# Kernel tuning notes

Measured on AMD Instinct MI355X. Metric: run time of the kernel, lower is better.

Reference implementation:

```python
import jax, jax.numpy as jnp
import numpy as np

NUM_HEADS = 8
HEAD_DIM = 64
HIDDEN_SIZE = 128
TOP_K = 16
EPS = 1e-6


def setup_inputs() -> dict:
    key = jax.random.key(0)
    k1, k2, k3 = jax.random.split(key, 3)
    B, H, S, D = 4, NUM_HEADS, 1024, HEAD_DIM
    return {
        "keys": jax.random.normal(k1, (B, H, S, D), dtype=jnp.float32),
        "values": jax.random.normal(k2, (B, H, S, D), dtype=jnp.float32),
        "queries": jax.random.normal(k3, (B, H, S, D), dtype=jnp.float32),
    }


def _project(x):
    # replicate [B,H,S,D] along last dim to cover HIDDEN_SIZE basis indices
    D = x.shape[-1]
    if D >= HIDDEN_SIZE:
        return x[..., :HIDDEN_SIZE]
    repeats = (HIDDEN_SIZE + D - 1) // D
    return jnp.tile(x, (1, 1, 1, repeats))[..., :HIDDEN_SIZE]


def reference(keys, values, queries):
    B, H, S, D = keys.shape
    b_idx = jnp.arange(B)[:, None, None]   # [B,1,1]
    h_idx = jnp.arange(H)[None, :, None]   # [1,H,1]

    # ---- update: scatter-add outer products into assigned memory bank ----
    assignments = jnp.argmax(jnp.abs(_project(keys)), axis=-1)  # [B,H,S]
    outer = values[..., :, None] * keys[..., None, :]           # [B,H,S,D,D] (v k^T)
    M = jnp.zeros((B, H, HIDDEN_SIZE, D, D), dtype=keys.dtype)
    M = M.at[b_idx, h_idx, assignments].add(outer)
    z = jnp.zeros((B, H, HIDDEN_SIZE, D), dtype=keys.dtype)
    z = z.at[b_idx, h_idx, assignments].add(keys)

    # ---- retrieve: top-k basis selection, gather-matvec, weighted combine ----
    scores = jnp.abs(_project(queries))                          # [B,H,S,HIDDEN]
    top_scores, top_idx = jax.lax.top_k(scores, TOP_K)           # [B,H,S,K]
    weights = jax.nn.softmax(top_scores, axis=-1)

    output = jnp.zeros((B, H, S, D), dtype=queries.dtype)
    for k in range(TOP_K):
        mem = top_idx[..., k]                                    # [B,H,S]
        M_sel = M[b_idx, h_idx, mem]                             # [B,H,S,D,D]
        z_sel = z[b_idx, h_idx, mem]                             # [B,H,S,D]
        num = jnp.einsum('bhsde,bhse->bhsd', M_sel, queries)
        den = jnp.einsum('bhsd,bhsd->bhs', z_sel, queries)[..., None] + EPS
        output = output + weights[..., k:k + 1] * (num / den)
    return output
```

## Files before the change

### kernel.cpp

```cpp
#include <hip/hip_runtime.h>
#include <math.h>

#define S_LEN 1024
#define EPS 1e-6f

typedef __attribute__((ext_vector_type(8)))  short bf16x8;
typedef __attribute__((ext_vector_type(4)))  short bf16x4;
typedef __attribute__((ext_vector_type(16))) float float16v;


__device__ __forceinline__ void bar_lgkm() {
    asm volatile("s_waitcnt lgkmcnt(0)" ::: "memory");
    __builtin_amdgcn_s_barrier();
    __builtin_amdgcn_sched_barrier(0);
    asm volatile("" ::: "memory");
}

#define PIN(x) asm volatile("" : "+v"(x))

__device__ __forceinline__ unsigned short f2bf(float f) {
    unsigned int u = __float_as_uint(f);
    unsigned int r = (u + 0x7fffu + ((u >> 16) & 1u)) >> 16;
    return (unsigned short)r;
}

__device__ __forceinline__ bf16x8 pack8(float4 a, float4 b) {
    bf16x8 r;
    r[0] = (short)f2bf(a.x); r[1] = (short)f2bf(a.y);
    r[2] = (short)f2bf(a.z); r[3] = (short)f2bf(a.w);
    r[4] = (short)f2bf(b.x); r[5] = (short)f2bf(b.y);
    r[6] = (short)f2bf(b.z); r[7] = (short)f2bf(b.w);
    return r;
}

__global__ __launch_bounds__(512) void k_pre(const float* __restrict__ keys,
                                             const float* __restrict__ queries,
                                             int* __restrict__ kcnt2,
                                             unsigned short* __restrict__ klist2,
                                             int* __restrict__ qcnt2,
                                             unsigned* __restrict__ qpair,
                                             unsigned char* __restrict__ qflag,
                                             float* __restrict__ out) {
    const int bh   = blockIdx.x >> 5;
    const int blk  = blockIdx.x & 31;
    const int wv   = threadIdx.x >> 6;
    const int lane = threadIdx.x & 63;

    __shared__ int khist[64], qhist[64];
    __shared__ alignas(16) unsigned rq_s[8][4][64];
    if (threadIdx.x < 64) { khist[threadIdx.x] = 0; qhist[threadIdx.x] = 0; }
    __syncthreads();

    const int s0 = blk * 32 + wv * 4;
    float kv[4], qv[4];
    #pragma unroll
    for (int i = 0; i < 4; ++i) {
        kv[i] = keys   [((size_t)bh * 1024 + s0 + i) * 64 + lane];
        qv[i] = queries[((size_t)bh * 1024 + s0 + i) * 64 + lane];
    }

    {
        float4 zz = {0.f, 0.f, 0.f, 0.f};
        float4* po = (float4*)(out + (size_t)blockIdx.x * 2048);
        po[threadIdx.x] = zz;
    }

    #pragma unroll
    for (int i = 0; i < 4; ++i) { PIN(kv[i]); PIN(qv[i]); }

    unsigned ud[4];
    #pragma unroll
    for (int i = 0; i < 4; ++i) {
        ud[i] = __float_as_uint(qv[i]) & 0x7fffffffu;
        rq_s[wv][i][lane] = ud[i];
    }

    float bv[4]; int bi[4];
    #pragma unroll
    for (int i = 0; i < 4; ++i) { bv[i] = fabsf(kv[i]); bi[i] = lane; }
    #pragma unroll
    for (int off = 1; off < 64; off <<= 1) {
        #pragma unroll
        for (int i = 0; i < 4; ++i) {
            float ov = __shfl_xor(bv[i], off, 64);
            int   oi = __shfl_xor(bi[i], off, 64);
            if (ov > bv[i] || (ov == bv[i] && oi < bi[i])) { bv[i] = ov; bi[i] = oi; }
        }
    }
    #pragma unroll
    for (int i = 0; i < 4; ++i) {
        if (lane == 0) {
            int pos = atomicAdd(&khist[bi[i]], 1);
            klist2[((size_t)bh * 64 + bi[i]) * 1024 + blk * 32 + pos] =
                (unsigned short)(s0 + i);
        }
    }

    int gt[4] = {0, 0, 0, 0};
    #pragma unroll
    for (int k4 = 0; k4 < 16; ++k4) {
        #pragma unroll
        for (int i = 0; i < 4; ++i) {
            const uint4 vv = *(const uint4*)&rq_s[wv][i][k4 * 4];
            gt[i] += (vv.x > ud[i]) ? 1 : 0;
            gt[i] += (vv.y > ud[i]) ? 1 : 0;
            gt[i] += (vv.z > ud[i]) ? 1 : 0;
            gt[i] += (vv.w > ud[i]) ? 1 : 0;
        }
    }
    int S[4];
    #pragma unroll
    for (int i = 0; i < 4; ++i) S[i] = gt[i];
    #pragma unroll
    for (int off = 1; off < 64; off <<= 1) {
        #pragma unroll
        for (int i = 0; i < 4; ++i) S[i] += __shfl_xor(S[i], off, 64);
    }
    float e[4];
    #pragma unroll
    for (int i = 0; i < 4; ++i) e[i] = expf(__uint_as_float(ud[i]));
    int copies[4], contrib[4], rank[4];
    #pragma unroll
    for (int i = 0; i < 4; ++i) {
        if (S[i] == 2016) {
            contrib[i] = (gt[i] < 8);
            copies[i]  = contrib[i] ? 2 : 0;
            rank[i]    = gt[i];
        } else {
            int eq = 0, eql = 0;
            #pragma unroll
            for (int k = 0; k < 64; ++k) {
                unsigned ui = (unsigned)__builtin_amdgcn_readlane((int)ud[i], k);
                eq  += (ui == ud[i]) ? 1 : 0;
                eql += (ui == ud[i] && k < lane) ? 1 : 0;
            }
            int pos_low  = 2 * gt[i] + eql;
            int pos_high = pos_low + eq;
            copies[i]  = (pos_low < 16 ? 1 : 0) + (pos_high < 16 ? 1 : 0);
            contrib[i] = (pos_low < 16);
            rank[i]    = 15;
        }
    }
    float ce[4];
    #pragma unroll
    for (int i = 0; i < 4; ++i) ce[i] = (float)copies[i] * e[i];
    #pragma unroll
    for (int off = 1; off < 64; off <<= 1) {
        #pragma unroll
        for (int i = 0; i < 4; ++i) ce[i] += __shfl_xor(ce[i], off, 64);
    }
    #pragma unroll
    for (int i = 0; i < 4; ++i) {
        if (contrib[i]) {
            int pos = atomicAdd(&qhist[lane], 1);
            unsigned wb = __float_as_uint(e[i] / ce[i]) & 0xFFFFC000u;
            qpair[((size_t)bh * 64 + lane) * 1024 + blk * 32 + pos] =
                wb | ((unsigned)rank[i] << 10) | (unsigned)(s0 + i);
        }
        if (qflag && lane == 0)
            qflag[bh * 1024 + s0 + i] = (S[i] == 2016) ? 0 : 1;
    }
    __syncthreads();
    if (threadIdx.x < 64) {
        kcnt2[(bh * 64 + threadIdx.x) * 32 + blk] = khist[threadIdx.x];
        qcnt2[(bh * 64 + threadIdx.x) * 32 + blk] = qhist[threadIdx.x];
    }
}

template <bool SC>
__global__ __launch_bounds__(256) void k_mainB(const float* __restrict__ keys,
                                               const float* __restrict__ values,
                                               const float* __restrict__ queries,
                                               const int* __restrict__ kcnt2,
                                               const unsigned short* __restrict__ klist2,
                                               const int* __restrict__ qcnt2,
                                               const unsigned* __restrict__ qpair,
                                               unsigned short* __restrict__ Obuf,
                                               float* __restrict__ out) {
    const int g     = blockIdx.x;
    const int bh    = g >> 6;
    const int bank  = g & 63;
    const int t     = threadIdx.x;
    const int lane  = t & 63;
    const int grp   = t >> 6;

    __shared__ alignas(16) unsigned short M_bf[64 * 64];
    __shared__ alignas(16) unsigned short Q_bf[64 * 64];
    __shared__ alignas(16) unsigned short Ou_bf[64 * 68];
    __shared__ unsigned short s_match[256];
    __shared__ unsigned q_ent[256];
    __shared__ int    koffs_s[33], qoffs_s[33];
    __shared__ float  z_s[64];
    __shared__ double den_s[64];
    __shared__ float  w_s[2][64];
    __shared__ int    sq_s[2][64];

    if (t < 64) {
        int i = t & 31;
        int c = (t < 32) ? kcnt2[(bh * 64 + bank) * 32 + i]
                         : qcnt2[(bh * 64 + bank) * 32 + i];
        #pragma unroll
        for (int off = 1; off < 32; off <<= 1) {
            int o = __shfl(c, t - off, 64);
            if (i >= off) c += o;
        }
        if (t < 32) { if (i == 0) koffs_s[0] = 0; koffs_s[i + 1] = c; }
        else        { if (i == 0) qoffs_s[0] = 0; qoffs_s[i + 1] = c; }
    }
    bar_lgkm();

    const int nq = qoffs_s[32];
    const int nm = koffs_s[32];
    if (nq == 0) return;
    if (nm == 0) {
        if constexpr (SC) {
            for (int jg = t; jg < nq; jg += 256) {
                int seg = 0;
                #pragma unroll
                for (int i = 1; i < 32; ++i) if (jg >= qoffs_s[i]) seg = i;
                unsigned e = qpair[(size_t)(bh * 64 + bank) * 1024 + seg * 32 +
                                   (jg - qoffs_s[seg])];
                int r = (e >> 10) & 15;
                if (r < 8) {
                    uint4 z4 = {0u, 0u, 0u, 0u};
                    uint4* dst = (uint4*)&Obuf[(((size_t)bh * 1024 +
                                 (e & 1023u)) * 8 + r) * 64];
                    #pragma unroll
                    for (int x = 0; x < 8; ++x) dst[x] = z4;
                }
            }
        }
        return;
    }

    {
        const int cn0 = min(256, nm);
        if (t < cn0) {
            int seg = 0;
            #pragma unroll
            for (int i = 1; i < 32; ++i) if (t >= koffs_s[i]) seg = i;
            s_match[t] = klist2[(size_t)(bh * 64 + bank) * 1024 + seg * 32 +
                                (t - koffs_s[seg])];
        }
        if (t < min(256, nq)) {
            int seg = 0;
            #pragma unroll
            for (int i = 1; i < 32; ++i) if (t >= qoffs_s[i]) seg = i;
            q_ent[t] = qpair[(size_t)(bh * 64 + bank) * 1024 + seg * 32 +
                             (t - qoffs_s[seg])];
        }
    }
    bar_lgkm();

    {
        float acc[16];
        #pragma unroll
        for (int m = 0; m < 16; ++m) acc[m] = 0.f;
        float zacc = 0.f;
        const float* kb = keys   + (size_t)bh * S_LEN * 64;
        const float* vb = values + (size_t)bh * S_LEN * 64;
        int it = 0;
        for (int cb = 0; cb < nm; cb += 256) {
            const int cn = min(256, nm - cb);
            if (cb > 0) {
                bar_lgkm();
                if (t < cn) {
                    int idx = cb + t;
                    int seg = 0;
                    #pragma unroll
                    for (int i = 1; i < 32; ++i) if (idx >= koffs_s[i]) seg = i;
                    s_match[t] = klist2[(size_t)(bh * 64 + bank) * 1024 +
                                        seg * 32 + (idx - koffs_s[seg])];
                }
                bar_lgkm();
            }
            for (int base = 0; base < cn; base += 8, ++it) {
                float* kst = (float*)Ou_bf + (it & 1) * 1024;
                float* vst = kst + 512;
                #pragma unroll
                for (int rr = 0; rr < 2; ++rr) {
                    int row = grp + rr * 4;
                    if (base + row < cn) {
                        int s = s_match[base + row];
                        kst[row * 64 + lane] = kb[(size_t)s * 64 + lane];
                        vst[row * 64 + lane] = vb[(size_t)s * 64 + lane];
                    }
                }
                bar_lgkm();
                int lim = min(8, cn - base);
                for (int jj = 0; jj < lim; ++jj) {
                    float kv = kst[jj * 64 + lane];
                    #pragma unroll
                    for (int m = 0; m < 16; ++m)
                        acc[m] += vst[jj * 64 + grp * 16 + m] * kv;
                }
                if (t < 64)
                    for (int jj = 0; jj < lim; ++jj) zacc += kst[jj * 64 + t];
            }
        }
        #pragma unroll
        for (int m = 0; m < 16; ++m) {
            int dv = grp * 16 + m;
            M_bf[dv * 64 + (((lane >> 3) ^ (dv & 7)) << 3) + (lane & 7)] = f2bf(acc[m]);
        }
        if (t < 64) z_s[t] = zacc;
    }
    bar_lgkm();

    const float* qb = queries + (size_t)bh * S_LEN * 64;
    float*       ob = out     + (size_t)bh * S_LEN * 64;
    unsigned short* obuf_b = SC ? Obuf + (size_t)bh * 1024 * 512 : nullptr;
    const int dvh = grp >> 1, jh = grp & 1;
    const int hi  = lane >> 5;
    const int jq  = t >> 2, cq = t & 3;

    int prev_nb = 0;
    bool have_pf = false;
    float4 f0, f1, f2, f3;
    unsigned pe = 0;
    for (int qloc = 0, batch = 0; qloc < nq; qloc += 64, ++batch) {
        const int nb  = min(64, nq - qloc);
        const int cur = batch & 1;

        if (qloc != 0 && (qloc & 255) == 0) {
            if (qloc + t < nq) {
                int jg = qloc + t;
                int seg = 0;
                #pragma unroll
                for (int i = 1; i < 32; ++i) if (jg >= qoffs_s[i]) seg = i;
                q_ent[t] = qpair[(size_t)(bh * 64 + bank) * 1024 + seg * 32 +
                                 (jg - qoffs_s[seg])];
            }
            bar_lgkm();
        }

        unsigned e = 0;
        const bool act = (jq < nb);
        if (act) {
            e = have_pf ? pe : q_ent[(qloc & 255) + jq];
            if (!have_pf) {
                const float4* src =
                    (const float4*)(qb + (size_t)(e & 1023u) * 64 + cq * 16);
                f0 = src[0]; f1 = src[1]; f2 = src[2]; f3 = src[3];
            }
        }

        if (batch > 0) {
            #pragma unroll
            for (int jj = 0; jj < 16; ++jj) {
                int j = grp * 16 + jj;
                if (j < prev_nb) {
                    unsigned short vb16 = Ou_bf[j * 68 + lane];
                    int sr = sq_s[1 - cur][j];
                    int s  = sr & 1023;
                    if constexpr (SC) {
                        int r = (sr >> 10) & 15;
                        if (r < 8)
                            obuf_b[((size_t)s * 8 + r) * 64 + lane] = vb16;
                        else
                            unsafeAtomicAdd(&ob[(size_t)s * 64 + lane],
                                __uint_as_float((unsigned)vb16 << 16));
                    } else {
                        unsafeAtomicAdd(&ob[(size_t)s * 64 + lane],
                            __uint_as_float((unsigned)vb16 << 16));
                    }
                }
            }
        }

        {
            bf16x8 p0 = {}, p1 = {};
            double d = 0.0;
            if (act) {
                if ((t & 3) == 0) {
                    sq_s[cur][jq] = (int)(e & 0x3FFFu);
                    w_s[cur][jq]  = __uint_as_float(e & 0xFFFFC000u);
                }
                p0 = pack8(f0, f1);
                p1 = pack8(f2, f3);
                const float4* zz4 = (const float4*)&z_s[cq * 16];
                float4 z0 = zz4[0], z1 = zz4[1], z2 = zz4[2], z3 = zz4[3];
                double da, db;
                da  = (double)z0.x * f0.x + (double)z0.y * f0.y + (double)z0.z * f0.z + (double)z0.w * f0.w;
                db  = (double)z1.x * f1.x + (double)z1.y * f1.y + (double)z1.z * f1.z + (double)z1.w * f1.w;
                da += (double)z2.x * f2.x + (double)z2.y * f2.y + (double)z2.z * f2.z + (double)z2.w * f2.w;
                db += (double)z3.x * f3.x + (double)z3.y * f3.y + (double)z3.z * f3.z + (double)z3.w * f3.w;
                d = da + db;
            }
            int c0 = cq * 2;
            *(bf16x8*)&Q_bf[jq * 64 + ((c0 ^ (jq & 7)) << 3)]       = p0;
            *(bf16x8*)&Q_bf[jq * 64 + (((c0 + 1) ^ (jq & 7)) << 3)] = p1;
            d += __shfl_xor(d, 1, 64);
            d += __shfl_xor(d, 2, 64);
            if ((t & 3) == 0) den_s[jq] = d;
        }

        {
            const int qn = qloc + 64;
            have_pf = false;
            if (qn < nq && (qn & 255) != 0) {
                int nbn = min(64, nq - qn);
                if (jq < nbn) {
                    pe = q_ent[(qn & 255) + jq];
                    const float4* src =
                        (const float4*)(qb + (size_t)(pe & 1023u) * 64 + cq * 16);
                    f0 = src[0]; f1 = src[1]; f2 = src[2]; f3 = src[3];
                    have_pf = true;
                }
            }
        }
        bar_lgkm();

        float16v C;
        #pragma unroll
        for (int i = 0; i < 16; ++i) C[i] = 0.f;
        const int am = dvh * 32 + (lane & 31);
        const int bn = jh  * 32 + (lane & 31);
        #pragma unroll
        for (int ks = 0; ks < 4; ++ks) {
            int ch = ks * 2 + hi;
            bf16x8 af = *(const bf16x8*)&M_bf[am * 64 + ((ch ^ (am & 7)) << 3)];
            bf16x8 bf = *(const bf16x8*)&Q_bf[bn * 64 + ((ch ^ (bn & 7)) << 3)];
            C = __builtin_amdgcn_mfma_f32_32x32x16_bf16(af, bf, C, 0, 0, 0);
        }
        {
            double den = den_s[bn];
            float  w   = w_s[cur][bn];
            float rinv = (float)((double)w / (den + (double)EPS));
            #pragma unroll
            for (int rq = 0; rq < 4; ++rq) {
                bf16x4 pk;
                pk[0] = (short)f2bf(C[rq * 4 + 0] * rinv);
                pk[1] = (short)f2bf(C[rq * 4 + 1] * rinv);
                pk[2] = (short)f2bf(C[rq * 4 + 2] * rinv);
                pk[3] = (short)f2bf(C[rq * 4 + 3] * rinv);
                *(bf16x4*)&Ou_bf[bn * 68 + dvh * 32 + rq * 8 + hi * 4] = pk;
            }
        }
        bar_lgkm();
        prev_nb = nb;
    }
    {
        const int cur = (((nq + 63) >> 6) - 1) & 1;
        #pragma unroll
        for (int jj = 0; jj < 16; ++jj) {
            int j = grp * 16 + jj;
            if (j < prev_nb) {
                unsigned short vb16 = Ou_bf[j * 68 + lane];
                int sr = sq_s[cur][j];
                int s  = sr & 1023;
                if constexpr (SC) {
                    int r = (sr >> 10) & 15;
                    if (r < 8)
                        obuf_b[((size_t)s * 8 + r) * 64 + lane] = vb16;
                    else
                        unsafeAtomicAdd(&ob[(size_t)s * 64 + lane],
                            __uint_as_float((unsigned)vb16 << 16));
                } else {
                    unsafeAtomicAdd(&ob[(size_t)s * 64 + lane],
                        __uint_as_float((unsigned)vb16 << 16));
                }
            }
        }
    }
}

__global__ __launch_bounds__(256) void k_reduce(const unsigned short* __restrict__ Obuf,
                                                const unsigned char* __restrict__ qflag,
                                                float* __restrict__ out) {
    const int wv   = threadIdx.x >> 6;
    const int lane = threadIdx.x & 63;
    const int q0   = (blockIdx.x * 4 + wv) * 8;
    #pragma unroll
    for (int i = 0; i < 8; ++i) {
        int q = q0 + i;
        if (qflag[q]) continue;
        const unsigned short* obr = Obuf + (size_t)q * 512;
        float acc = 0.f;
        #pragma unroll
        for (int r = 0; r < 8; ++r)
            acc += __uint_as_float((unsigned)obr[r * 64 + lane] << 16);
        out[(size_t)q * 64 + lane] = acc;
    }
}

extern "C" void kernel_launch(void* const* d_in, const int* in_sizes, int n_in,
                              void* d_out, int out_size, void* d_ws, size_t ws_size,
                              hipStream_t stream) {
    const float* keys    = (const float*)d_in[0];
    const float* values  = (const float*)d_in[1];
    const float* queries = (const float*)d_in[2];
    char* ws = (char*)d_ws;
    int*            kcnt2  = (int*)(ws);
    int*            qcnt2  = (int*)(ws + 262144);
    unsigned short* klist2 = (unsigned short*)(ws + 524288);
    unsigned*       qpair  = (unsigned*)(ws + 4718592);
    unsigned char*  qflag  = (unsigned char*)(ws + 30416896);
    unsigned short* Obuf   = (unsigned short*)(ws + 30449664);
    const bool big2 = (ws_size >= 64004096u);

    k_pre<<<1024, 512, 0, stream>>>(keys, queries, kcnt2, klist2, qcnt2, qpair,
                                    big2 ? qflag : nullptr, (float*)d_out);
    if (big2) {
        k_mainB<true><<<2048, 256, 0, stream>>>(keys, values, queries, kcnt2,
                                                klist2, qcnt2, qpair, Obuf,
                                                (float*)d_out);
        k_reduce<<<1024, 256, 0, stream>>>(Obuf, qflag, (float*)d_out);
    } else {
        k_mainB<false><<<2048, 256, 0, stream>>>(keys, values, queries, kcnt2,
                                                 klist2, qcnt2, qpair, Obuf,
                                                 (float*)d_out);
    }
}
```

Measured before the change: 132.7 us.

## Replace per-bank outer-product memory build with attention-style QK^T·V MFMA factorization

Instead of building the 64x64 memory matrix M per bank through scalar FMA outer-product accumulation, the kernel now computes scores S = K·Q^T on MFMA over 32-key chunks, scales them by weight/denominator, and multiplies by V^T, again on MFMA. Queries are processed in batches of 128 rather than 64, and z is accumulated directly from global memory. This removes the scalar outer-product loop but adds per-chunk key/value staging and barriers, so the work now scales with the number of matched keys times the number of queries. The old query prefetch and double-buffered metadata are dropped.

Result: slower. 154.9 us (+16.7%).

```diff
diff --git a/kernel.cpp b/kernel.cpp
--- a/kernel.cpp
+++ b/kernel.cpp
@@ -183,17 +183,20 @@
     const int t     = threadIdx.x;
     const int lane  = t & 63;
     const int grp   = t >> 6;
-
-    __shared__ alignas(16) unsigned short M_bf[64 * 64];
-    __shared__ alignas(16) unsigned short Q_bf[64 * 64];
-    __shared__ alignas(16) unsigned short Ou_bf[64 * 68];
+    const int hi    = lane >> 5;
+    const int l31   = lane & 31;
+
+    __shared__ alignas(16) unsigned short K_bf[32 * 64];
+    __shared__ alignas(16) unsigned short VT_bf[64 * 40];
+    __shared__ alignas(16) unsigned short QO[128 * 72];
+    __shared__ alignas(16) unsigned short P_bf[128 * 40];
     __shared__ unsigned short s_match[256];
     __shared__ unsigned q_ent[256];
     __shared__ int    koffs_s[33], qoffs_s[33];
     __shared__ float  z_s[64];
-    __shared__ double den_s[64];
-    __shared__ float  w_s[2][64];
-    __shared__ int    sq_s[2][64];
+    __shared__ double den_s[128];
+    __shared__ float  w_s[128];
+    __shared__ int    sq_s[128];
 
     if (t < 64) {
         int i = t & 31;
@@ -212,14 +215,14 @@
     const int nq = qoffs_s[32];
     const int nm = koffs_s[32];
     if (nq == 0) return;
+    const size_t listbase = (size_t)(bh * 64 + bank) * 1024;
     if (nm == 0) {
         if constexpr (SC) {
             for (int jg = t; jg < nq; jg += 256) {
                 int seg = 0;
                 #pragma unroll
                 for (int i = 1; i < 32; ++i) if (jg >= qoffs_s[i]) seg = i;
-                unsigned e = qpair[(size_t)(bh * 64 + bank) * 1024 + seg * 32 +
-                                   (jg - qoffs_s[seg])];
+                unsigned e = qpair[listbase + seg * 32 + (jg - qoffs_s[seg])];
                 int r = (e >> 10) & 15;
                 if (r < 8) {
                     uint4 z4 = {0u, 0u, 0u, 0u};
@@ -233,125 +236,119 @@
         return;
     }
 
+    const float* kb = keys    + (size_t)bh * S_LEN * 64;
+    const float* vb = values  + (size_t)bh * S_LEN * 64;
+    const float* qb = queries + (size_t)bh * S_LEN * 64;
+
+    if (t < min(256, nm)) {
+        int seg = 0;
+        #pragma unroll
+        for (int i = 1; i < 32; ++i) if (t >= koffs_s[i]) seg = i;
+        s_match[t] = klist2[listbase + seg * 32 + (t - koffs_s[seg])];
+    }
+    if (t < min(256, nq)) {
+        int seg = 0;
+        #pragma unroll
+        for (int i = 1; i < 32; ++i) if (t >= qoffs_s[i]) seg = i;
+        q_ent[t] = qpair[listbase + seg * 32 + (t - qoffs_s[seg])];
+    }
+    bar_lgkm();
+
+    int win = 0;
+
     {
-        const int cn0 = min(256, nm);
-        if (t < cn0) {
-            int seg = 0;
-            #pragma unroll
-            for (int i = 1; i < 32; ++i) if (t >= koffs_s[i]) seg = i;
-            s_match[t] = klist2[(size_t)(bh * 64 + bank) * 1024 + seg * 32 +
-                                (t - koffs_s[seg])];
-        }
-        if (t < min(256, nq)) {
-            int seg = 0;
-            #pragma unroll
-            for (int i = 1; i < 32; ++i) if (t >= qoffs_s[i]) seg = i;
-            q_ent[t] = qpair[(size_t)(bh * 64 + bank) * 1024 + seg * 32 +
-                             (t - qoffs_s[seg])];
-        }
-    }
-    bar_lgkm();
-
-    {
-        float acc[16];
-        #pragma unroll
-        for (int m = 0; m < 16; ++m) acc[m] = 0.f;
-        float zacc = 0.f;
-        const float* kb = keys   + (size_t)bh * S_LEN * 64;
-        const float* vb = values + (size_t)bh * S_LEN * 64;
-        int it = 0;
+        float* zp4 = (float*)P_bf;
+        float zp = 0.f;
         for (int cb = 0; cb < nm; cb += 256) {
-            const int cn = min(256, nm - cb);
+            int cn = min(256, nm - cb);
             if (cb > 0) {
                 bar_lgkm();
                 if (t < cn) {
-                    int idx = cb + t;
-                    int seg = 0;
+                    int idx = cb + t, seg = 0;
                     #pragma unroll
                     for (int i = 1; i < 32; ++i) if (idx >= koffs_s[i]) seg = i;
-                    s_match[t] = klist2[(size_t)(bh * 64 + bank) * 1024 +
-                                        seg * 32 + (idx - koffs_s[seg])];
+                    s_match[t] = klist2[listbase + seg * 32 + (idx - koffs_s[seg])];
                 }
                 bar_lgkm();
-            }
-            for (int base = 0; base < cn; base += 8, ++it) {
-                float* kst = (float*)Ou_bf + (it & 1) * 1024;
-                float* vst = kst + 512;
+                win = cb;
+            }
+            for (int r = grp; r < cn; r += 4)
+                zp += kb[(size_t)s_match[r] * 64 + lane];
+        }
+        zp4[grp * 64 + lane] = zp;
+        bar_lgkm();
+        if (t < 64) z_s[t] = zp4[t] + zp4[64 + t] + zp4[128 + t] + zp4[192 + t];
+    }
+
+    const int kchunks = (nm + 31) >> 5;
+
+    auto ensure_win = [&](int c0) {
+        int need = c0 & ~255;
+        if (need != win) {
+            bar_lgkm();
+            int cn = min(256, nm - need);
+            if (t < cn) {
+                int idx = need + t, seg = 0;
                 #pragma unroll
-                for (int rr = 0; rr < 2; ++rr) {
-                    int row = grp + rr * 4;
-                    if (base + row < cn) {
-                        int s = s_match[base + row];
-                        kst[row * 64 + lane] = kb[(size_t)s * 64 + lane];
-                        vst[row * 64 + lane] = vb[(size_t)s * 64 + lane];
-                    }
-                }
-                bar_lgkm();
-                int lim = min(8, cn - base);
-                for (int jj = 0; jj < lim; ++jj) {
-                    float kv = kst[jj * 64 + lane];
-                    #pragma unroll
-                    for (int m = 0; m < 16; ++m)
-                        acc[m] += vst[jj * 64 + grp * 16 + m] * kv;
-                }
-                if (t < 64)
-                    for (int jj = 0; jj < lim; ++jj) zacc += kst[jj * 64 + t];
-            }
-        }
-        #pragma unroll
-        for (int m = 0; m < 16; ++m) {
-            int dv = grp * 16 + m;
-            M_bf[dv * 64 + (((lane >> 3) ^ (dv & 7)) << 3) + (lane & 7)] = f2bf(acc[m]);
-        }
-        if (t < 64) z_s[t] = zacc;
-    }
+                for (int i = 1; i < 32; ++i) if (idx >= koffs_s[i]) seg = i;
+                s_match[t] = klist2[listbase + seg * 32 + (idx - koffs_s[seg])];
+            }
+            bar_lgkm();
+            win = need;
+        }
+    };
+
+    auto stage_kv = [&](int kc) {
+        int c0 = kc * 32, cnt = min(32, nm - c0);
+        int r = t >> 3, c8 = t & 7;
+        float4 ka = {0,0,0,0}, ka2 = {0,0,0,0}, va = {0,0,0,0}, va2 = {0,0,0,0};
+        if (r < cnt) {
+            int s = s_match[(c0 - win) + r];
+            const float4* ks = (const float4*)(kb + (size_t)s * 64 + c8 * 8);
+            ka = ks[0]; ka2 = ks[1];
+            const float4* vs = (const float4*)(vb + (size_t)s * 64 + c8 * 8);
+            va = vs[0]; va2 = vs[1];
+        }
+        *(bf16x8*)&K_bf[r * 64 + ((c8 ^ (r & 7)) << 3)] = pack8(ka, ka2);
+        VT_bf[(c8 * 8 + 0) * 40 + r] = f2bf(va.x);
+        VT_bf[(c8 * 8 + 1) * 40 + r] = f2bf(va.y);
+        VT_bf[(c8 * 8 + 2) * 40 + r] = f2bf(va.z);
+        VT_bf[(c8 * 8 + 3) * 40 + r] = f2bf(va.w);
+        VT_bf[(c8 * 8 + 4) * 40 + r] = f2bf(va2.x);
+        VT_bf[(c8 * 8 + 5) * 40 + r] = f2bf(va2.y);
+        VT_bf[(c8 * 8 + 6) * 40 + r] = f2bf(va2.z);
+        VT_bf[(c8 * 8 + 7) * 40 + r] = f2bf(va2.w);
+    };
+
+    if (kchunks == 1) { ensure_win(0); stage_kv(0); }
     bar_lgkm();
 
-    const float* qb = queries + (size_t)bh * S_LEN * 64;
-    float*       ob = out     + (size_t)bh * S_LEN * 64;
-    unsigned short* obuf_b = SC ? Obuf + (size_t)bh * 1024 * 512 : nullptr;
-    const int dvh = grp >> 1, jh = grp & 1;
-    const int hi  = lane >> 5;
-    const int jq  = t >> 2, cq = t & 3;
+    const int qn_ = grp * 32 + l31;
 
     int prev_nb = 0;
-    bool have_pf = false;
-    float4 f0, f1, f2, f3;
-    unsigned pe = 0;
-    for (int qloc = 0, batch = 0; qloc < nq; qloc += 64, ++batch) {
-        const int nb  = min(64, nq - qloc);
-        const int cur = batch & 1;
-
-        if (qloc != 0 && (qloc & 255) == 0) {
-            if (qloc + t < nq) {
-                int jg = qloc + t;
-                int seg = 0;
+    for (int qb0 = 0, batch = 0; qb0 < nq; qb0 += 128, ++batch) {
+        const int nb = min(128, nq - qb0);
+
+        if (qb0 != 0 && (qb0 & 255) == 0) {
+            bar_lgkm();
+            if (qb0 + t < nq) {
+                int jg = qb0 + t, seg = 0;
                 #pragma unroll
                 for (int i = 1; i < 32; ++i) if (jg >= qoffs_s[i]) seg = i;
-                q_ent[t] = qpair[(size_t)(bh * 64 + bank) * 1024 + seg * 32 +
-                                 (jg - qoffs_s[seg])];
+                q_ent[t] = qpair[listbase + seg * 32 + (jg - qoffs_s[seg])];
             }
             bar_lgkm();
         }
 
-        unsigned e = 0;
-        const bool act = (jq < nb);
-        if (act) {
-            e = have_pf ? pe : q_ent[(qloc & 255) + jq];
-            if (!have_pf) {
-                const float4* src =
-                    (const float4*)(qb + (size_t)(e & 1023u) * 64 + cq * 16);
-                f0 = src[0]; f1 = src[1]; f2 = src[2]; f3 = src[3];
-            }
-        }
-
         if (batch > 0) {
+            float* ob = out + (size_t)bh * S_LEN * 64;
+            unsigned short* obuf_b = SC ? Obuf + (size_t)bh * 1024 * 512 : nullptr;
             #pragma unroll
-            for (int jj = 0; jj < 16; ++jj) {
-                int j = grp * 16 + jj;
+            for (int jj = 0; jj < 32; ++jj) {
+                int j = grp * 32 + jj;
                 if (j < prev_nb) {
-                    unsigned short vb16 = Ou_bf[j * 68 + lane];
-                    int sr = sq_s[1 - cur][j];
+                    unsigned short vb16 = QO[j * 72 + lane];
+                    int sr = sq_s[j];
                     int s  = sr & 1023;
                     if constexpr (SC) {
                         int r = (sr >> 10) & 15;
@@ -366,16 +363,23 @@
                     }
                 }
             }
-        }
-
-        {
+            bar_lgkm();
+        }
+
+        #pragma unroll
+        for (int h = 0; h < 2; ++h) {
+            int j = h * 64 + (t >> 2), cq = t & 3;
             bf16x8 p0 = {}, p1 = {};
             double d = 0.0;
-            if (act) {
+            if (j < nb) {
+                unsigned e = q_ent[(qb0 + j) & 255];
                 if ((t & 3) == 0) {
-                    sq_s[cur][jq] = (int)(e & 0x3FFFu);
-                    w_s[cur][jq]  = __uint_as_float(e & 0xFFFFC000u);
+                    sq_s[j] = (int)(e & 0x3FFFu);
+                    w_s[j]  = __uint_as_float(e & 0xFFFFC000u);
                 }
+                const float4* src =
+                    (const float4*)(qb + (size_t)(e & 1023u) * 64 + cq * 16);
+                float4 f0 = src[0], f1 = src[1], f2 = src[2], f3 = src[3];
                 p0 = pack8(f0, f1);
                 p1 = pack8(f2, f3);
                 const float4* zz4 = (const float4*)&z_s[cq * 16];
@@ -388,66 +392,88 @@
                 d = da + db;
             }
             int c0 = cq * 2;
-            *(bf16x8*)&Q_bf[jq * 64 + ((c0 ^ (jq & 7)) << 3)]       = p0;
-            *(bf16x8*)&Q_bf[jq * 64 + (((c0 + 1) ^ (jq & 7)) << 3)] = p1;
+            *(bf16x8*)&QO[j * 72 + ((c0 ^ (j & 7)) << 3)]       = p0;
+            *(bf16x8*)&QO[j * 72 + (((c0 + 1) ^ (j & 7)) << 3)] = p1;
             d += __shfl_xor(d, 1, 64);
             d += __shfl_xor(d, 2, 64);
-            if ((t & 3) == 0) den_s[jq] = d;
-        }
-
-        {
-            const int qn = qloc + 64;
-            have_pf = false;
-            if (qn < nq && (qn & 255) != 0) {
-                int nbn = min(64, nq - qn);
-                if (jq < nbn) {
-                    pe = q_ent[(qn & 255) + jq];
-                    const float4* src =
-                        (const float4*)(qb + (size_t)(pe & 1023u) * 64 + cq * 16);
-                    f0 = src[0]; f1 = src[1]; f2 = src[2]; f3 = src[3];
-                    have_pf = true;
+            if ((t & 3) == 0) den_s[j] = d;
+        }
+        bar_lgkm();
+
+        float16v C0, C1;
+        #pragma unroll
+        for (int i = 0; i < 16; ++i) { C0[i] = 0.f; C1[i] = 0.f; }
+
+        for (int kc = 0; kc < kchunks; ++kc) {
+            if (kchunks > 1) {
+                bar_lgkm();
+                ensure_win(kc * 32);
+                stage_kv(kc);
+                bar_lgkm();
+            }
+            float16v Sv;
+            #pragma unroll
+            for (int i = 0; i < 16; ++i) Sv[i] = 0.f;
+            #pragma unroll
+            for (int ks = 0; ks < 4; ++ks) {
+                int ch = ks * 2 + hi;
+                bf16x8 af = *(const bf16x8*)&K_bf[l31 * 64 + ((ch ^ (l31 & 7)) << 3)];
+                bf16x8 bf = *(const bf16x8*)&QO[qn_ * 72 + ((ch ^ (qn_ & 7)) << 3)];
+                Sv = __builtin_amdgcn_mfma_f32_32x32x16_bf16(af, bf, Sv, 0, 0, 0);
+            }
+            {
+                double den = den_s[qn_];
+                float  w   = w_s[qn_];
+                float rinv = (float)((double)w / (den + (double)EPS));
+                #pragma unroll
+                for (int rq = 0; rq < 4; ++rq) {
+                    bf16x4 pk;
+                    pk[0] = (short)f2bf(Sv[rq * 4 + 0] * rinv);
+                    pk[1] = (short)f2bf(Sv[rq * 4 + 1] * rinv);
+                    pk[2] = (short)f2bf(Sv[rq * 4 + 2] * rinv);
+                    pk[3] = (short)f2bf(Sv[rq * 4 + 3] * rinv);
+                    *(bf16x4*)&P_bf[qn_ * 40 + rq * 8 + hi * 4] = pk;
                 }
             }
-        }
-        bar_lgkm();
-
-        float16v C;
-        #pragma unroll
-        for (int i = 0; i < 16; ++i) C[i] = 0.f;
-        const int am = dvh * 32 + (lane & 31);
-        const int bn = jh  * 32 + (lane & 31);
-        #pragma unroll
-        for (int ks = 0; ks < 4; ++ks) {
-            int ch = ks * 2 + hi;
-            bf16x8 af = *(const bf16x8*)&M_bf[am * 64 + ((ch ^ (am & 7)) << 3)];
-            bf16x8 bf = *(const bf16x8*)&Q_bf[bn * 64 + ((ch ^ (bn & 7)) << 3)];
-            C = __builtin_amdgcn_mfma_f32_32x32x16_bf16(af, bf, C, 0, 0, 0);
-        }
-        {
-            double den = den_s[bn];
-            float  w   = w_s[cur][bn];
-            float rinv = (float)((double)w / (den + (double)EPS));
+            bar_lgkm();
             #pragma unroll
-            for (int rq = 0; rq < 4; ++rq) {
-                bf16x4 pk;
-                pk[0] = (short)f2bf(C[rq * 4 + 0] * rinv);
-                pk[1] = (short)f2bf(C[rq * 4 + 1] * rinv);
-                pk[2] = (short)f2bf(C[rq * 4 + 2] * rinv);
-                pk[3] = (short)f2bf(C[rq * 4 + 3] * rinv);
-                *(bf16x4*)&Ou_bf[bn * 68 + dvh * 32 + rq * 8 + hi * 4] = pk;
-            }
+            for (int ks2 = 0; ks2 < 2; ++ks2) {
+                int ch2 = ks2 * 2 + hi;
+                bf16x8 pf  = *(const bf16x8*)&P_bf[qn_ * 40 + ch2 * 8];
+                bf16x8 af0 = *(const bf16x8*)&VT_bf[l31 * 40 + ch2 * 8];
+                C0 = __builtin_amdgcn_mfma_f32_32x32x16_bf16(af0, pf, C0, 0, 0, 0);
+                bf16x8 af1 = *(const bf16x8*)&VT_bf[(32 + l31) * 40 + ch2 * 8];
+                C1 = __builtin_amdgcn_mfma_f32_32x32x16_bf16(af1, pf, C1, 0, 0, 0);
+            }
+        }
+
+        #pragma unroll
+        for (int rq = 0; rq < 4; ++rq) {
+            bf16x4 pk0, pk1;
+            pk0[0] = (short)f2bf(C0[rq * 4 + 0]);
+            pk0[1] = (short)f2bf(C0[rq * 4 + 1]);
+            pk0[2] = (short)f2bf(C0[rq * 4 + 2]);
+            pk0[3] = (short)f2bf(C0[rq * 4 + 3]);
+            *(bf16x4*)&QO[qn_ * 72 + rq * 8 + hi * 4] = pk0;
+            pk1[0] = (short)f2bf(C1[rq * 4 + 0]);
+            pk1[1] = (short)f2bf(C1[rq * 4 + 1]);
+            pk1[2] = (short)f2bf(C1[rq * 4 + 2]);
+            pk1[3] = (short)f2bf(C1[rq * 4 + 3]);
+            *(bf16x4*)&QO[qn_ * 72 + 32 + rq * 8 + hi * 4] = pk1;
         }
         bar_lgkm();
         prev_nb = nb;
     }
+
     {
-        const int cur = (((nq + 63) >> 6) - 1) & 1;
-        #pragma unroll
-        for (int jj = 0; jj < 16; ++jj) {
-            int j = grp * 16 + jj;
+        float* ob = out + (size_t)bh * S_LEN * 64;
+        unsigned short* obuf_b = SC ? Obuf + (size_t)bh * 1024 * 512 : nullptr;
+        #pragma unroll
+        for (int jj = 0; jj < 32; ++jj) {
+            int j = grp * 32 + jj;
             if (j < prev_nb) {
-                unsigned short vb16 = Ou_bf[j * 68 + lane];
-                int sr = sq_s[cur][j];
+                unsigned short vb16 = QO[j * 72 + lane];
+                int sr = sq_s[j];
                 int s  = sr & 1023;
                 if constexpr (SC) {
                     int r = (sr >> 10) & 15;
```
